# Kernel tuning notes

Measured on AMD Instinct MI355X. Metric: run time of the kernel, lower is better.

## Reference

```python
import jax, jax.numpy as jnp
import numpy as np

N, M = 50000, 16
NODE_DIM, EDGE_DIM = 128, 64
CONCAT_DIM = 2 * NODE_DIM + EDGE_DIM  # 320
LN_EPS = 1e-6  # flax.linen.LayerNorm default


def setup_inputs() -> dict:
    key = jax.random.key(0)
    ks = jax.random.split(key, 5)
    x = jax.random.normal(ks[0], (N, NODE_DIM), dtype=jnp.float32)
    nbr_fea = jax.random.normal(ks[1], (N, M, EDGE_DIM), dtype=jnp.float32)
    nbr_fea_idx = jax.random.randint(ks[2], (N, M), 0, N)
    ln_scale = jnp.ones((NODE_DIM,), dtype=jnp.float32)
    ln_bias = jnp.zeros((NODE_DIM,), dtype=jnp.float32)
    # lecun_normal-ish init scaled by fan-in (flax Dense default is lecun_normal)
    W1 = jax.random.normal(ks[3], (CONCAT_DIM, NODE_DIM), dtype=jnp.float32) / np.sqrt(CONCAT_DIM)
    b1 = jnp.zeros((NODE_DIM,), dtype=jnp.float32)
    W2 = jax.random.normal(ks[4], (NODE_DIM, NODE_DIM), dtype=jnp.float32) / np.sqrt(NODE_DIM)
    b2 = jnp.zeros((NODE_DIM,), dtype=jnp.float32)
    return {"x": x, "nbr_fea": nbr_fea, "nbr_fea_idx": nbr_fea_idx,
            "ln_scale": ln_scale, "ln_bias": ln_bias,
            "W1": W1, "b1": b1, "W2": W2, "b2": b2}


def _layer_norm(x, scale, bias):
    mu = jnp.mean(x, axis=-1, keepdims=True)
    var = jnp.mean(jnp.square(x - mu), axis=-1, keepdims=True)
    return (x - mu) * jax.lax.rsqrt(var + LN_EPS) * scale + bias


def reference(x, nbr_fea, nbr_fea_idx, ln_scale, ln_bias, W1, b1, W2, b2):
    # x: [N, D], nbr_fea: [N, M, E], nbr_fea_idx: [N, M]
    x_normed = _layer_norm(x, ln_scale, ln_bias)                 # [N, D]
    x_nbr = jnp.take(x_normed, nbr_fea_idx, axis=0)              # [N, M, D]
    m = nbr_fea_idx.shape[1]
    x_center = jnp.broadcast_to(x_normed[:, None, :], (x.shape[0], m, x.shape[1]))
    concat = jnp.concatenate([x_center, x_nbr, nbr_fea], axis=-1)  # [N, M, 2D+E]
    h = jax.nn.silu(jnp.einsum('nmc,cd->nmd', concat, W1) + b1)   # [N, M, D]
    msg = jnp.einsum('nmd,de->nme', h, W2) + b2                   # [N, M, D]
    agg = jnp.sum(msg, axis=1)                                    # [N, D]
    return x + agg
```

## Files before the change

kernel.cpp:

```cpp
#include <hip/hip_runtime.h>
#include <math.h>

#define N_NODES 50000
#define M_NBR 16
#define D 128
#define E 64

typedef __attribute__((ext_vector_type(8))) __bf16 bf16x8;
typedef __attribute__((ext_vector_type(4))) float f32x4;


__global__ __launch_bounds__(256) void k_prep(const float* __restrict__ W1,
                                              const float* __restrict__ W2,
                                              __bf16* __restrict__ w1a_f,
                                              __bf16* __restrict__ w1b_f,
                                              __bf16* __restrict__ w1c_f,
                                              __bf16* __restrict__ w2_f) {
  const int t = blockIdx.x * 256 + threadIdx.x;
  if (t < 16384) {
    const int j = t & 7, r = (t >> 3) & 15, c = (t >> 7) & 3, q = t >> 9;
    const int kt = q & 3, dt = q >> 2;
    w1a_f[t] = (__bf16)W1[(kt * 32 + c * 8 + j) * 128 + dt * 16 + r];
  } else if (t < 32768) {
    const int u = t - 16384;
    const int j = u & 7, r = (u >> 3) & 15, c = (u >> 7) & 3, q = u >> 9;
    const int kt = q & 3, dt = q >> 2;
    w1b_f[u] = (__bf16)W1[(128 + kt * 32 + c * 8 + j) * 128 + dt * 16 + r];
  } else if (t < 40960) {
    const int u = t - 32768;
    const int j = u & 7, r = (u >> 3) & 15, c = (u >> 7) & 3, q = u >> 9;
    const int kt = q & 1, dt = q >> 1;
    w1c_f[u] = (__bf16)W1[(256 + kt * 32 + c * 8 + j) * 128 + dt * 16 + r];
  } else if (t < 57344) {
    const int u = t - 40960;
    const int j = u & 7, r = (u >> 3) & 15, c = (u >> 7) & 3, q = u >> 9;
    const int kt = q & 3, dt = q >> 2;
    const int i = kt * 32 + c * 8 + j;
    const int ak = (i & 7) * 16 + (i >> 3);
    w2_f[u] = (__bf16)W2[ak * 128 + dt * 16 + r];
  }
}

__global__ __launch_bounds__(256) void k_t12f(const float* __restrict__ x,
                                              const float* __restrict__ sc,
                                              const float* __restrict__ bi,
                                              const __bf16* __restrict__ w1a_f,
                                              const __bf16* __restrict__ w1b_f,
                                              const float* __restrict__ b1,
                                              float* __restrict__ t1p,
                                              __bf16* __restrict__ t2bp) {
  const int wave = blockIdx.x * 4 + (threadIdx.x >> 6);
  if (wave >= N_NODES / 16) return;
  const int lane = threadIdx.x & 63;
  const int r = lane & 15, c = lane >> 4;
  const int node0 = wave * 16;

  const float* row = x + (size_t)(node0 + r) * 128 + c * 8;
  f32x4 va[8];
  #pragma unroll
  for (int kt = 0; kt < 4; ++kt) {
    va[2 * kt]     = *(const f32x4*)(row + kt * 32);
    va[2 * kt + 1] = *(const f32x4*)(row + kt * 32 + 4);
  }
  float s = 0.f;
  #pragma unroll
  for (int q = 0; q < 8; ++q) s += va[q][0] + va[q][1] + va[q][2] + va[q][3];
  s += __shfl_xor(s, 16, 64);
  s += __shfl_xor(s, 32, 64);
  const float mu = s * (1.0f / 128.0f);
  float qs = 0.f;
  #pragma unroll
  for (int q = 0; q < 8; ++q) {
    #pragma unroll
    for (int e = 0; e < 4; ++e) { const float dxx = va[q][e] - mu; qs += dxx * dxx; }
  }
  qs += __shfl_xor(qs, 16, 64);
  qs += __shfl_xor(qs, 32, 64);
  const float rs = rsqrtf(qs * (1.0f / 128.0f) + 1e-6f);

  bf16x8 af[4];
  #pragma unroll
  for (int kt = 0; kt < 4; ++kt) {
    const f32x4 s_lo = *(const f32x4*)(sc + kt * 32 + c * 8);
    const f32x4 s_hi = *(const f32x4*)(sc + kt * 32 + c * 8 + 4);
    const f32x4 b_lo = *(const f32x4*)(bi + kt * 32 + c * 8);
    const f32x4 b_hi = *(const f32x4*)(bi + kt * 32 + c * 8 + 4);
    #pragma unroll
    for (int e = 0; e < 4; ++e) {
      af[kt][e]     = (__bf16)(((va[2 * kt][e]     - mu) * rs) * s_lo[e] + b_lo[e]);
      af[kt][4 + e] = (__bf16)(((va[2 * kt + 1][e] - mu) * rs) * s_hi[e] + b_hi[e]);
    }
  }

  const bf16x8* wa = (const bf16x8*)w1a_f;
  const bf16x8* wb = (const bf16x8*)w1b_f;
  f32x4 acc1[8], acc2[8];
  #pragma unroll
  for (int dt = 0; dt < 8; ++dt) { acc1[dt] = (f32x4){0,0,0,0}; acc2[dt] = (f32x4){0,0,0,0}; }
  #pragma unroll
  for (int dt = 0; dt < 8; ++dt) {
    #pragma unroll
    for (int kt = 0; kt < 4; ++kt) {
      const bf16x8 bfa = wa[(dt * 4 + kt) * 64 + c * 16 + r];
      acc1[dt] = __builtin_amdgcn_mfma_f32_16x16x32_bf16(af[kt], bfa, acc1[dt], 0, 0, 0);
      const bf16x8 bfb = wb[(dt * 4 + kt) * 64 + c * 16 + r];
      acc2[dt] = __builtin_amdgcn_mfma_f32_16x16x32_bf16(af[kt], bfb, acc2[dt], 0, 0, 0);
    }
  }

  float b1v[8];
  #pragma unroll
  for (int dt = 0; dt < 8; ++dt) b1v[dt] = b1[dt * 16 + r];
  #pragma unroll
  for (int j = 0; j < 4; ++j) {
    const int node = node0 + c * 4 + j;
    f32x4 t1lo, t1hi;
    bf16x8 t2v;
    #pragma unroll
    for (int dt = 0; dt < 4; ++dt)  t1lo[dt]     = acc1[dt][j] + b1v[dt];
    #pragma unroll
    for (int dt = 4; dt < 8; ++dt)  t1hi[dt - 4] = acc1[dt][j] + b1v[dt];
    #pragma unroll
    for (int dt = 0; dt < 8; ++dt)  t2v[dt] = (__bf16)acc2[dt][j];
    *(f32x4*)(t1p + (size_t)node * 128 + r * 8)     = t1lo;
    *(f32x4*)(t1p + (size_t)node * 128 + r * 8 + 4) = t1hi;
    *(bf16x8*)(t2bp + (size_t)node * 128 + r * 8)   = t2v;
  }
}

struct NL {
  f32x4 lo0, hi0, lo1, hi1;
  bf16x8 tg0, tg1, tg2, tg3;
  f32x4 t1lo, t1hi;
};

__device__ __forceinline__ NL load_node(const float* __restrict__ nbr,
                                        const float* __restrict__ t1p,
                                        const __bf16* __restrict__ t2bp,
                                        int n, int4 g, int r, int c) {
  NL v;
  const float* arow = nbr + (size_t)n * (M_NBR * E) + r * E + c * 8;
  v.lo0 = *(const f32x4*)(arow);
  v.hi0 = *(const f32x4*)(arow + 4);
  v.lo1 = *(const f32x4*)(arow + 32);
  v.hi1 = *(const f32x4*)(arow + 36);
  v.tg0 = *(const bf16x8*)(t2bp + (size_t)g.x * 128 + r * 8);
  v.tg1 = *(const bf16x8*)(t2bp + (size_t)g.y * 128 + r * 8);
  v.tg2 = *(const bf16x8*)(t2bp + (size_t)g.z * 128 + r * 8);
  v.tg3 = *(const bf16x8*)(t2bp + (size_t)g.w * 128 + r * 8);
  v.t1lo = *(const f32x4*)(t1p + (size_t)n * 128 + r * 8);
  v.t1hi = *(const f32x4*)(t1p + (size_t)n * 128 + r * 8 + 4);
  return v;
}

__device__ __forceinline__ void compute_node(const NL& v,
                                             const bf16x8 (&bfrag)[8][2],
                                             int n, int lane, int r,
                                             float* __restrict__ hsum_p) {
  bf16x8 af0, af1;
  #pragma unroll
  for (int e = 0; e < 4; ++e) {
    af0[e] = (__bf16)v.lo0[e]; af0[4 + e] = (__bf16)v.hi0[e];
    af1[e] = (__bf16)v.lo1[e]; af1[4 + e] = (__bf16)v.hi1[e];
  }
  f32x4 acc[8];
  #pragma unroll
  for (int dt = 0; dt < 8; ++dt) acc[dt] = (f32x4){0, 0, 0, 0};
  #pragma unroll
  for (int dt = 0; dt < 8; ++dt) {
    acc[dt] = __builtin_amdgcn_mfma_f32_16x16x32_bf16(af0, bfrag[dt][0], acc[dt], 0, 0, 0);
    acc[dt] = __builtin_amdgcn_mfma_f32_16x16x32_bf16(af1, bfrag[dt][1], acc[dt], 0, 0, 0);
  }
  float ssum[8];
  #pragma unroll
  for (int dt = 0; dt < 8; ++dt) {
    const float tb = (dt < 4) ? v.t1lo[dt & 3] : v.t1hi[dt & 3];
    float s = 0.f;
    { const float h = acc[dt][0] + tb + (float)v.tg0[dt]; s += __fdividef(h, 1.0f + __expf(-h)); }
    { const float h = acc[dt][1] + tb + (float)v.tg1[dt]; s += __fdividef(h, 1.0f + __expf(-h)); }
    { const float h = acc[dt][2] + tb + (float)v.tg2[dt]; s += __fdividef(h, 1.0f + __expf(-h)); }
    { const float h = acc[dt][3] + tb + (float)v.tg3[dt]; s += __fdividef(h, 1.0f + __expf(-h)); }
    s += __shfl_xor(s, 16, 64);
    s += __shfl_xor(s, 32, 64);
    ssum[dt] = s;
  }
  if (lane < 16) {
    f32x4 o_lo, o_hi;
    #pragma unroll
    for (int dt = 0; dt < 4; ++dt) { o_lo[dt] = ssum[dt]; o_hi[dt] = ssum[dt + 4]; }
    *(f32x4*)(hsum_p + (size_t)n * 128 + r * 8)     = o_lo;
    *(f32x4*)(hsum_p + (size_t)n * 128 + r * 8 + 4) = o_hi;
  }
}

__global__ __launch_bounds__(256, 2) void k_edge(const float* __restrict__ nbr,
                                                 const int* __restrict__ idx,
                                                 const float* __restrict__ t1p,
                                                 const __bf16* __restrict__ t2bp,
                                                 const __bf16* __restrict__ w1c_f,
                                                 float* __restrict__ hsum_p) {
  const int lane = threadIdx.x & 63;
  const int wid  = threadIdx.x >> 6;
  const int r = lane & 15, c = lane >> 4;

  const bf16x8* wc = (const bf16x8*)w1c_f;
  bf16x8 bfrag[8][2];
  #pragma unroll
  for (int dt = 0; dt < 8; ++dt) {
    bfrag[dt][0] = wc[(dt * 2 + 0) * 64 + c * 16 + r];
    bfrag[dt][1] = wc[(dt * 2 + 1) * 64 + c * 16 + r];
  }

  const int node0 = (blockIdx.x * 4 + wid) * 4;
  const int4 g0 = *(const int4*)(idx + (node0 + 0) * M_NBR + c * 4);
  const int4 g1 = *(const int4*)(idx + (node0 + 1) * M_NBR + c * 4);
  const int4 g2 = *(const int4*)(idx + (node0 + 2) * M_NBR + c * 4);
  const int4 g3 = *(const int4*)(idx + (node0 + 3) * M_NBR + c * 4);

  NL a = load_node(nbr, t1p, t2bp, node0 + 0, g0, r, c);
  NL b = load_node(nbr, t1p, t2bp, node0 + 1, g1, r, c);
  __builtin_amdgcn_sched_barrier(0);
  compute_node(a, bfrag, node0 + 0, lane, r, hsum_p);

  a = load_node(nbr, t1p, t2bp, node0 + 2, g2, r, c);
  __builtin_amdgcn_sched_barrier(0);
  compute_node(b, bfrag, node0 + 1, lane, r, hsum_p);

  b = load_node(nbr, t1p, t2bp, node0 + 3, g3, r, c);
  __builtin_amdgcn_sched_barrier(0);
  compute_node(a, bfrag, node0 + 2, lane, r, hsum_p);
  compute_node(b, bfrag, node0 + 3, lane, r, hsum_p);
}

__global__ __launch_bounds__(256) void k_out(const float* __restrict__ hsum_p,
                                             const __bf16* __restrict__ w2_f,
                                             const float* __restrict__ b2,
                                             const float* __restrict__ x,
                                             float* __restrict__ out) {
  const int wave = blockIdx.x * 4 + (threadIdx.x >> 6);
  if (wave >= N_NODES / 16) return;
  const int lane = threadIdx.x & 63;
  const int r = lane & 15, c = lane >> 4;
  const int node0 = wave * 16;

  const float* row = hsum_p + (size_t)(node0 + r) * 128 + c * 8;
  bf16x8 af[4];
  #pragma unroll
  for (int kt = 0; kt < 4; ++kt) {
    const f32x4 lo = *(const f32x4*)(row + kt * 32);
    const f32x4 hi = *(const f32x4*)(row + kt * 32 + 4);
    #pragma unroll
    for (int e = 0; e < 4; ++e) { af[kt][e] = (__bf16)lo[e]; af[kt][4 + e] = (__bf16)hi[e]; }
  }

  const bf16x8* w2 = (const bf16x8*)w2_f;
  f32x4 acc[8];
  #pragma unroll
  for (int dt = 0; dt < 8; ++dt) acc[dt] = (f32x4){0,0,0,0};
  #pragma unroll
  for (int dt = 0; dt < 8; ++dt) {
    #pragma unroll
    for (int kt = 0; kt < 4; ++kt) {
      const bf16x8 bf = w2[(dt * 4 + kt) * 64 + c * 16 + r];
      acc[dt] = __builtin_amdgcn_mfma_f32_16x16x32_bf16(af[kt], bf, acc[dt], 0, 0, 0);
    }
  }

  float b2v[8];
  #pragma unroll
  for (int dt = 0; dt < 8; ++dt) b2v[dt] = 16.0f * b2[dt * 16 + r];
  #pragma unroll
  for (int j = 0; j < 4; ++j) {
    const int node = node0 + c * 4 + j;
    #pragma unroll
    for (int dt = 0; dt < 8; ++dt) {
      const size_t o = (size_t)node * 128 + dt * 16 + r;
      out[o] = x[o] + acc[dt][j] + b2v[dt];
    }
  }
}

extern "C" void kernel_launch(void* const* d_in, const int* in_sizes, int n_in,
                              void* d_out, int out_size, void* d_ws, size_t ws_size,
                              hipStream_t stream) {
  const float* x        = (const float*)d_in[0];
  const float* nbr_fea  = (const float*)d_in[1];
  const int*   nbr_idx  = (const int*)d_in[2];
  const float* ln_scale = (const float*)d_in[3];
  const float* ln_bias  = (const float*)d_in[4];
  const float* W1       = (const float*)d_in[5];
  const float* b1       = (const float*)d_in[6];
  const float* W2       = (const float*)d_in[7];
  const float* b2       = (const float*)d_in[8];
  float* out = (float*)d_out;

  char* ws = (char*)d_ws;
  float*  t1p    = (float*)(ws);
  float*  hsum_p = (float*)(ws + 25600000);
  __bf16* t2bp   = (__bf16*)(ws + 51200000);
  __bf16* w1a_f  = (__bf16*)(ws + 64000000);
  __bf16* w1b_f  = (__bf16*)(ws + 64032768);
  __bf16* w1c_f  = (__bf16*)(ws + 64065536);
  __bf16* w2_f   = (__bf16*)(ws + 64081920);

  k_prep <<<224, 256, 0, stream>>>(W1, W2, w1a_f, w1b_f, w1c_f, w2_f);
  k_t12f <<<(N_NODES / 16 + 3) / 4, 256, 0, stream>>>(x, ln_scale, ln_bias,
                                                      w1a_f, w1b_f, b1, t1p, t2bp);
  k_edge <<<N_NODES / 16, 256, 0, stream>>>(nbr_fea, nbr_idx, t1p, t2bp, w1c_f, hsum_p);
  k_out  <<<(N_NODES / 16 + 3) / 4, 256, 0, stream>>>(hsum_p, w2_f, b2, x, out);
}
```

Baseline: 141.7 us.

## Stage edge features into LDS via async global_load_lds double buffering

The edge kernel now streams each node's neighbour-feature tile into per-wave LDS double buffers using asynchronous global-to-LDS loads, with explicit vmcnt waits so the next node's tile is in flight while the current one is computed. The gathered t2/t1 loads are split out and issued separately, and the block size drops to 128 threads with a new launch-bounds occupancy hint. The aim is to cut register pressure from holding raw fp32 features and to raise memory-level parallelism on the dominant nbr_fea stream. The cost is an extra LDS round trip and hand-placed wait counts that rely on in-order vmcnt accounting.

```diff
diff --git a/kernel.cpp b/kernel.cpp
--- a/kernel.cpp
+++ b/kernel.cpp
@@ -8,6 +8,19 @@
 
 typedef __attribute__((ext_vector_type(8))) __bf16 bf16x8;
 typedef __attribute__((ext_vector_type(4))) float f32x4;
+
+__device__ __forceinline__ void gload16(const void* g, void* l) {
+  __builtin_amdgcn_global_load_lds(
+      (const __attribute__((address_space(1))) void*)g,
+      (__attribute__((address_space(3))) void*)l, 16, 0, 0);
+}
+
+#define SB() __builtin_amdgcn_sched_barrier(0)
+#if __has_builtin(__builtin_amdgcn_s_waitcnt)
+#define VMWAIT(N) do { SB(); __builtin_amdgcn_s_waitcnt(0x3F70 | (N)); SB(); } while (0)
+#else
+#define VMWAIT(N) do { SB(); asm volatile("s_waitcnt vmcnt(" #N ")" ::: "memory"); SB(); } while (0)
+#endif
 
 
 __global__ __launch_bounds__(256) void k_prep(const float* __restrict__ W1,
@@ -128,22 +141,15 @@
   }
 }
 
-struct NL {
-  f32x4 lo0, hi0, lo1, hi1;
+struct TG {
   bf16x8 tg0, tg1, tg2, tg3;
   f32x4 t1lo, t1hi;
 };
 
-__device__ __forceinline__ NL load_node(const float* __restrict__ nbr,
-                                        const float* __restrict__ t1p,
-                                        const __bf16* __restrict__ t2bp,
-                                        int n, int4 g, int r, int c) {
-  NL v;
-  const float* arow = nbr + (size_t)n * (M_NBR * E) + r * E + c * 8;
-  v.lo0 = *(const f32x4*)(arow);
-  v.hi0 = *(const f32x4*)(arow + 4);
-  v.lo1 = *(const f32x4*)(arow + 32);
-  v.hi1 = *(const f32x4*)(arow + 36);
+__device__ __forceinline__ TG load_tg(const float* __restrict__ t1p,
+                                      const __bf16* __restrict__ t2bp,
+                                      int n, int4 g, int r) {
+  TG v;
   v.tg0 = *(const bf16x8*)(t2bp + (size_t)g.x * 128 + r * 8);
   v.tg1 = *(const bf16x8*)(t2bp + (size_t)g.y * 128 + r * 8);
   v.tg2 = *(const bf16x8*)(t2bp + (size_t)g.z * 128 + r * 8);
@@ -153,15 +159,29 @@
   return v;
 }
 
-__device__ __forceinline__ void compute_node(const NL& v,
+__device__ __forceinline__ void stageA(const float* __restrict__ nbr,
+                                       int n, int r, int c, char* buf) {
+  const char* an = (const char*)nbr + (size_t)n * 4096 + r * 256 + c * 32;
+  gload16(an +   0, buf +    0);
+  gload16(an +  16, buf + 1024);
+  gload16(an + 128, buf + 2048);
+  gload16(an + 144, buf + 3072);
+}
+
+__device__ __forceinline__ void compute_node(const char* buf, const TG& v,
                                              const bf16x8 (&bfrag)[8][2],
                                              int n, int lane, int r,
                                              float* __restrict__ hsum_p) {
+  const f32x4 lo0 = *(const f32x4*)(buf +    0 + lane * 16);
+  const f32x4 hi0 = *(const f32x4*)(buf + 1024 + lane * 16);
+  const f32x4 lo1 = *(const f32x4*)(buf + 2048 + lane * 16);
+  const f32x4 hi1 = *(const f32x4*)(buf + 3072 + lane * 16);
+
   bf16x8 af0, af1;
   #pragma unroll
   for (int e = 0; e < 4; ++e) {
-    af0[e] = (__bf16)v.lo0[e]; af0[4 + e] = (__bf16)v.hi0[e];
-    af1[e] = (__bf16)v.lo1[e]; af1[4 + e] = (__bf16)v.hi1[e];
+    af0[e] = (__bf16)lo0[e]; af0[4 + e] = (__bf16)hi0[e];
+    af1[e] = (__bf16)lo1[e]; af1[4 + e] = (__bf16)hi1[e];
   }
   f32x4 acc[8];
   #pragma unroll
@@ -193,15 +213,18 @@
   }
 }
 
-__global__ __launch_bounds__(256, 2) void k_edge(const float* __restrict__ nbr,
+__global__ __launch_bounds__(128, 3) void k_edge(const float* __restrict__ nbr,
                                                  const int* __restrict__ idx,
                                                  const float* __restrict__ t1p,
                                                  const __bf16* __restrict__ t2bp,
                                                  const __bf16* __restrict__ w1c_f,
                                                  float* __restrict__ hsum_p) {
+  __shared__ char smem[2 * 2 * 4096];
   const int lane = threadIdx.x & 63;
   const int wid  = threadIdx.x >> 6;
   const int r = lane & 15, c = lane >> 4;
+  char* bufA = smem + wid * 8192;
+  char* bufB = bufA + 4096;
 
   const bf16x8* wc = (const bf16x8*)w1c_f;
   bf16x8 bfrag[8][2];
@@ -211,25 +234,34 @@
     bfrag[dt][1] = wc[(dt * 2 + 1) * 64 + c * 16 + r];
   }
 
-  const int node0 = (blockIdx.x * 4 + wid) * 4;
+  const int node0 = (blockIdx.x * 2 + wid) * 4;
   const int4 g0 = *(const int4*)(idx + (node0 + 0) * M_NBR + c * 4);
   const int4 g1 = *(const int4*)(idx + (node0 + 1) * M_NBR + c * 4);
   const int4 g2 = *(const int4*)(idx + (node0 + 2) * M_NBR + c * 4);
   const int4 g3 = *(const int4*)(idx + (node0 + 3) * M_NBR + c * 4);
 
-  NL a = load_node(nbr, t1p, t2bp, node0 + 0, g0, r, c);
-  NL b = load_node(nbr, t1p, t2bp, node0 + 1, g1, r, c);
-  __builtin_amdgcn_sched_barrier(0);
-  compute_node(a, bfrag, node0 + 0, lane, r, hsum_p);
-
-  a = load_node(nbr, t1p, t2bp, node0 + 2, g2, r, c);
-  __builtin_amdgcn_sched_barrier(0);
-  compute_node(b, bfrag, node0 + 1, lane, r, hsum_p);
-
-  b = load_node(nbr, t1p, t2bp, node0 + 3, g3, r, c);
-  __builtin_amdgcn_sched_barrier(0);
-  compute_node(a, bfrag, node0 + 2, lane, r, hsum_p);
-  compute_node(b, bfrag, node0 + 3, lane, r, hsum_p);
+  stageA(nbr, node0 + 0, r, c, bufA);
+  TG t0 = load_tg(t1p, t2bp, node0 + 0, g0, r);
+  SB();
+  stageA(nbr, node0 + 1, r, c, bufB);
+  VMWAIT(4);
+  compute_node(bufA, t0, bfrag, node0 + 0, lane, r, hsum_p);
+
+  TG t1v = load_tg(t1p, t2bp, node0 + 1, g1, r);
+  SB();
+  stageA(nbr, node0 + 2, r, c, bufA);
+  VMWAIT(4);
+  compute_node(bufB, t1v, bfrag, node0 + 1, lane, r, hsum_p);
+
+  TG t2g = load_tg(t1p, t2bp, node0 + 2, g2, r);
+  SB();
+  stageA(nbr, node0 + 3, r, c, bufB);
+  VMWAIT(4);
+  compute_node(bufA, t2g, bfrag, node0 + 2, lane, r, hsum_p);
+
+  TG t3g = load_tg(t1p, t2bp, node0 + 3, g3, r);
+  VMWAIT(0);
+  compute_node(bufB, t3g, bfrag, node0 + 3, lane, r, hsum_p);
 }
 
 __global__ __launch_bounds__(256) void k_out(const float* __restrict__ hsum_p,
@@ -306,6 +338,6 @@
   k_prep <<<224, 256, 0, stream>>>(W1, W2, w1a_f, w1b_f, w1c_f, w2_f);
   k_t12f <<<(N_NODES / 16 + 3) / 4, 256, 0, stream>>>(x, ln_scale, ln_bias,
                                                       w1a_f, w1b_f, b1, t1p, t2bp);
-  k_edge <<<N_NODES / 16, 256, 0, stream>>>(nbr_fea, nbr_idx, t1p, t2bp, w1c_f, hsum_p);
+  k_edge <<<N_NODES / 8, 128, 0, stream>>>(nbr_fea, nbr_idx, t1p, t2bp, w1c_f, hsum_p);
   k_out  <<<(N_NODES / 16 + 3) / 4, 256, 0, stream>>>(hsum_p, w2_f, b2, x, out);
 }
```

New measurement: 131.1 us. -7.5%, faster.
